# Kernel tuning notes

Hardware: AMD Instinct MI355X
Metric: run time of the kernel (lower is better)

Reference implementation:

```python
import jax, jax.numpy as jnp
import numpy as np

B, S, D, A_DIM = 8, 2048, 256, 64

def setup_inputs() -> dict:
    key = jax.random.key(0)
    k_x, k_wm, k_wl, k_eps = jax.random.split(key, 4)
    return {
        "x": jax.random.normal(k_x, (B, S, D), dtype=jnp.float32),
        "W_mean": jax.random.normal(k_wm, (D, A_DIM), dtype=jnp.float32) * (1.0 / np.sqrt(D)),
        "b_mean": jnp.zeros((A_DIM,), dtype=jnp.float32),
        "W_logvar": jax.random.normal(k_wl, (D, A_DIM), dtype=jnp.float32) * (1.0 / np.sqrt(D)),
        "b_logvar": jnp.zeros((A_DIM,), dtype=jnp.float32),
        "eps": jax.random.normal(k_eps, (B, S, A_DIM), dtype=jnp.float32),
    }

def reference(x, W_mean, b_mean, W_logvar, b_logvar, eps):
    d = x.shape[-1]
    scale = 1.0 / jnp.sqrt(jnp.asarray(d, dtype=x.dtype))
    # S_det = x x^T / sqrt(d)  -> [B, S, S]
    scores = jnp.einsum("bsd,btd->bst", x, x) * scale
    attn = jax.nn.softmax(scores, axis=-1)
    # A_det = softmax(S) x  -> [B, S, D]
    A_det = jnp.einsum("bst,btd->bsd", attn, x)
    A_mean = A_det @ W_mean + b_mean        # [B, S, A_DIM]
    A_logvar = A_det @ W_logvar + b_logvar  # [B, S, A_DIM]
    A = A_mean + jnp.exp(0.5 * A_logvar) * eps  # sqrt(exp(logvar)) = exp(logvar/2)
    return (A_mean, A_logvar, A)
```

## Files before the change

kernel.cpp:

```cpp
#include <hip/hip_runtime.h>

#define B_ 8
#define S_ 2048
#define D_ 256

typedef _Float16 f16;
typedef f16 f16x2 __attribute__((ext_vector_type(2)));
typedef f16 f16x8 __attribute__((ext_vector_type(8)));
typedef float f32x16 __attribute__((ext_vector_type(16)));
typedef unsigned int u32;
typedef u32 u32x4 __attribute__((ext_vector_type(4)));

typedef const __attribute__((address_space(1))) unsigned int* gptr_t;
typedef __attribute__((address_space(3))) unsigned int* lptr_t;

__device__ __forceinline__ void gload_lds16(const void* g, void* l) {
  __builtin_amdgcn_global_load_lds((gptr_t)(unsigned long long)g,
                                   (lptr_t)(unsigned long long)l, 16, 0, 0);
}

__device__ __forceinline__ u32 packf16(float a, float b) {
  f16x2 t; t[0] = (f16)a; t[1] = (f16)b;
  return __builtin_bit_cast(u32, t);
}

__device__ __forceinline__ void pack16(const f32x16& p, int hi, u32x4& o0, u32x4& o1) {
#pragma unroll
  for (int c2 = 0; c2 < 2; ++c2) {
    u32 a1 = packf16(p[8 * c2 + 0], p[8 * c2 + 1]);
    u32 a2 = packf16(p[8 * c2 + 2], p[8 * c2 + 3]);
    u32 b1 = packf16(p[8 * c2 + 4], p[8 * c2 + 5]);
    u32 b2 = packf16(p[8 * c2 + 6], p[8 * c2 + 7]);
    u32 xa1 = __shfl_xor(a1, 32), xa2 = __shfl_xor(a2, 32);
    u32 xb1 = __shfl_xor(b1, 32), xb2 = __shfl_xor(b2, 32);
    u32x4 f;
    f[0] = hi ? xb1 : a1;
    f[1] = hi ? xb2 : a2;
    f[2] = hi ? b1 : xa1;
    f[3] = hi ? b2 : xa2;
    if (c2) o1 = f; else o0 = f;
  }
}

#define SC2F 0.09016844f
#define NMAXR 20.0f

__global__ void prep(const float* __restrict__ x, const float* __restrict__ Wm,
                     const float* __restrict__ Wl, f16* __restrict__ xh,
                     float* __restrict__ n2, f16* __restrict__ Wt) {
  __shared__ f16 tile[64][264];
  const int bid = blockIdx.x;
  const int t = threadIdx.x;
  if (bid < 256) {
    const int b = bid >> 5, st = bid & 31;
    const int s0 = st * 64;
    const float* xb = x + ((size_t)(b * S_ + s0)) * D_;
    f16* xhb = xh + ((size_t)(b * S_ + s0)) * D_;
#pragma unroll
    for (int it = 0; it < 16; ++it) {
      int flat = it * 256 + t;
      int r = flat >> 6, c4 = flat & 63;
      float4 v = *reinterpret_cast<const float4*>(xb + r * 256 + c4 * 4);
      f16 h0 = (f16)v.x, h1 = (f16)v.y, h2 = (f16)v.z, h3 = (f16)v.w;
      f16x2 p0 = {h0, h1}, p1 = {h2, h3};
      uint2 wv; wv.x = __builtin_bit_cast(u32, p0); wv.y = __builtin_bit_cast(u32, p1);
      *reinterpret_cast<uint2*>(xhb + r * 256 + c4 * 4) = wv;
      tile[r][c4 * 4 + 0] = h0; tile[r][c4 * 4 + 1] = h1;
      tile[r][c4 * 4 + 2] = h2; tile[r][c4 * 4 + 3] = h3;
    }
    __syncthreads();
    {
      int r = t >> 2, qd = t & 3;
      float s = 0.0f;
#pragma unroll
      for (int i = 0; i < 8; ++i) {
        f16x8 v = *reinterpret_cast<const f16x8*>(&tile[r][qd * 64 + i * 8]);
#pragma unroll
        for (int u = 0; u < 8; ++u) { float f = (float)v[u]; s += f * f; }
      }
      s += __shfl_xor(s, 1); s += __shfl_xor(s, 2);
      if (qd == 0) n2[b * S_ + s0 + r] = s;
    }
  } else {
    int idx = (bid - 256) * 1024 + t * 4;
    int j = idx >> 8, d = idx & 255;
#pragma unroll
    for (int k2 = 0; k2 < 4; ++k2) {
      float v = (j < 64) ? Wm[(d + k2) * 64 + j] : Wl[(d + k2) * 64 + (j - 64)];
      Wt[idx + k2] = (f16)v;
    }
  }
}

__launch_bounds__(256)
__global__ void xw_kern(const f16* __restrict__ xh, const f16* __restrict__ Wt,
                        f16* __restrict__ XWt) {
  __shared__ f16 Ax[2][4096];
  __shared__ f16 Ww[2][8192];
  const int idx = blockIdx.x;
  const int b = idx & 7;
  const int sb = (idx >> 3) * 64;
  const int tid = threadIdx.x, lane = tid & 63, w = tid >> 6;
  const int l31 = lane & 31, hi = lane >> 5;
  const f16* xb = xh + (size_t)b * S_ * D_;

#define XW_STAGE(st, pp)                                                       \
  {                                                                            \
    _Pragma("unroll") for (int i = 0; i < 2; ++i) {                            \
      int ch = i * 256 + tid; int r = ch >> 3, c = ch & 7;                     \
      int csrc = c ^ (r & 7);                                                  \
      gload_lds16(xb + (size_t)(sb + r) * 256 + ((st) * 64) + csrc * 8,        \
                  &Ax[(pp)][0] + ch * 8);                                      \
    }                                                                          \
    _Pragma("unroll") for (int i = 0; i < 4; ++i) {                            \
      int ch = i * 256 + tid; int r = ch >> 3, c = ch & 7;                     \
      int csrc = c ^ (r & 7);                                                  \
      gload_lds16(Wt + (size_t)r * 256 + ((st) * 64) + csrc * 8,               \
                  &Ww[(pp)][0] + ch * 8);                                      \
    }                                                                          \
  }

  f32x16 acc[2];
#pragma unroll
  for (int i = 0; i < 2; ++i)
#pragma unroll
    for (int e = 0; e < 16; ++e) acc[i][e] = 0.0f;

  XW_STAGE(0, 0);
  __syncthreads();
#pragma unroll
  for (int t = 0; t < 4; ++t) {
    const int p = t & 1;
    if (t < 3) XW_STAGE(t + 1, p ^ 1);
#pragma unroll
    for (int kc = 0; kc < 4; ++kc) {
      int cc = ((2 * kc + hi) ^ (l31 & 7)) * 8;
      f16x8 bf = *reinterpret_cast<const f16x8*>(&Ww[p][(w * 32 + l31) * 64 + cc]);
#pragma unroll
      for (int mi = 0; mi < 2; ++mi) {
        f16x8 af = *reinterpret_cast<const f16x8*>(&Ax[p][(mi * 32 + l31) * 64 + cc]);
        acc[mi] = __builtin_amdgcn_mfma_f32_32x32x16_f16(af, bf, acc[mi], 0, 0, 0);
      }
    }
    __syncthreads();
  }
#undef XW_STAGE

  const int j = w * 32 + l31;
  f16* dst = XWt + ((size_t)b * 128 + j) * 2048;
#pragma unroll
  for (int mi = 0; mi < 2; ++mi) {
    u32x4 s0, s1;
    pack16(acc[mi], hi, s0, s1);
    *reinterpret_cast<u32x4*>(dst + sb + mi * 32 + hi * 8) = s0;
    *reinterpret_cast<u32x4*>(dst + sb + mi * 32 + 16 + hi * 8) = s1;
  }
}

__launch_bounds__(512, 4)
__global__ void gemm1_kern(const f16* __restrict__ xh, const float* __restrict__ n2,
                           f16* __restrict__ P, float* __restrict__ Lp,
                           int b0, int bm, int bsh) {
  __shared__ __align__(16) char smem[65536];
  f16* Aq = (f16*)smem;
  f16* Bk = (f16*)(smem + 32768);
  const int idx = blockIdx.x;
  const int bl = idx & bm;
  int tdec = idx >> bsh;
  int qt = 0;
#pragma unroll 1
  while (tdec >= 16 - qt) { tdec -= 16 - qt; ++qt; }
  const int kt = qt + tdec;
  const int b = b0 + bl;
  const int qb = qt * 128, kb = kt * 128;
  const int tid = threadIdx.x, lane = tid & 63, w = tid >> 6;
  const int l31 = lane & 31, hi = lane >> 5;
  const int wq = w >> 2, wk = w & 3;
  const f16* xb = xh + (size_t)b * S_ * D_;

#define G1_STAGE(st, pp)                                                       \
  { _Pragma("unroll") for (int i = 0; i < 4; ++i) {                            \
      int ii = w * 4 + i;                                                      \
      int flat = ii * 64 + lane;                                               \
      bool isB = ii >= 16;                                                     \
      int ch = isB ? flat - 1024 : flat;                                       \
      int r = ch >> 3, c = ch & 7;                                             \
      int csrc = c ^ (r & 7);                                                  \
      const f16* src = xb + (size_t)((isB ? kb : qb) + r) * 256 +              \
                       (st) * 64 + csrc * 8;                                   \
      f16* dst = (isB ? Bk : Aq) + ((pp) * 8192) + ch * 8;                     \
      gload_lds16(src, dst);                                                   \
    } }

  f32x16 acc[2];
#pragma unroll
  for (int i = 0; i < 2; ++i)
#pragma unroll
    for (int e = 0; e < 16; ++e) acc[i][e] = 0.0f;

  G1_STAGE(0, 0);
  __syncthreads();
#pragma unroll
  for (int t = 0; t < 4; ++t) {
    const int p = t & 1;
    if (t < 3) G1_STAGE(t + 1, p ^ 1);
#pragma unroll
    for (int kc = 0; kc < 4; ++kc) {
      int cc = ((2 * kc + hi) ^ (l31 & 7)) * 8;
      f16x8 af  = *reinterpret_cast<const f16x8*>(Bk + p * 8192 + (wk * 32 + l31) * 64 + cc);
      f16x8 bf0 = *reinterpret_cast<const f16x8*>(Aq + p * 8192 + (wq * 64 + l31) * 64 + cc);
      f16x8 bf1 = *reinterpret_cast<const f16x8*>(Aq + p * 8192 + (wq * 64 + 32 + l31) * 64 + cc);
      acc[0] = __builtin_amdgcn_mfma_f32_32x32x16_f16(af, bf0, acc[0], 0, 0, 0);
      acc[1] = __builtin_amdgcn_mfma_f32_32x32x16_f16(af, bf1, acc[1], 0, 0, 0);
    }
    __syncthreads();
  }
#undef G1_STAGE

  float* raw = (float*)smem;
  if (kt != qt) {
#pragma unroll
    for (int ni = 0; ni < 2; ++ni)
#pragma unroll
      for (int j = 0; j < 16; ++j) {
        int kvloc = wk * 32 + (j & 3) + 8 * (j >> 2) + 4 * hi;
        int qloc = wq * 64 + ni * 32 + l31;
        raw[kvloc * 128 + (qloc ^ ((kvloc & 7) << 2))] = acc[ni][j];
      }
  }

  float r2[2], lsum[2];
  int qrow[2];
#pragma unroll
  for (int ni = 0; ni < 2; ++ni) {
    qrow[ni] = qb + wq * 64 + ni * 32 + l31;
    r2[ni] = sqrtf(n2[b * S_ + qrow[ni]]) * (NMAXR * SC2F);
    lsum[ni] = 0.0f;
  }
#pragma unroll
  for (int ni = 0; ni < 2; ++ni)
#pragma unroll
    for (int j = 0; j < 16; ++j) {
      float v = exp2f(acc[ni][j] * SC2F - r2[ni]);
      acc[ni][j] = v;
      lsum[ni] += v;
    }
#pragma unroll
  for (int ni = 0; ni < 2; ++ni) lsum[ni] += __shfl_xor(lsum[ni], 32);

  const int colb = kb + wk * 32;
#pragma unroll
  for (int ni = 0; ni < 2; ++ni) {
    u32x4 s0, s1;
    pack16(acc[ni], hi, s0, s1);
    size_t rowp = (size_t)(bl * S_ + qrow[ni]) * 2048;
    *reinterpret_cast<u32x4*>(P + rowp + colb + hi * 8) = s0;
    *reinterpret_cast<u32x4*>(P + rowp + colb + 16 + hi * 8) = s1;
  }

  if (kt != qt) {
    __syncthreads();
    const int kvr = tid >> 2;
    const int qseg = (tid & 3) * 32;
    float r2kv = sqrtf(n2[b * S_ + kb + kvr]) * (NMAXR * SC2F);
    u32 ow[16];
    float tsum = 0.0f;
#pragma unroll
    for (int c8 = 0; c8 < 8; ++c8) {
      int qs = qseg + c8 * 4;
      float4 v = *reinterpret_cast<const float4*>(
          &raw[kvr * 128 + (qs ^ ((kvr & 7) << 2))]);
      float e0 = exp2f(v.x * SC2F - r2kv), e1 = exp2f(v.y * SC2F - r2kv);
      float e2 = exp2f(v.z * SC2F - r2kv), e3 = exp2f(v.w * SC2F - r2kv);
      tsum += (e0 + e1) + (e2 + e3);
      ow[c8 * 2 + 0] = packf16(e0, e1);
      ow[c8 * 2 + 1] = packf16(e2, e3);
    }
    size_t rowp = (size_t)(bl * S_ + kb + kvr) * 2048;
#pragma unroll
    for (int sseg = 0; sseg < 4; ++sseg) {
      u32x4 sv;
      sv[0] = ow[sseg * 4 + 0]; sv[1] = ow[sseg * 4 + 1];
      sv[2] = ow[sseg * 4 + 2]; sv[3] = ow[sseg * 4 + 3];
      *reinterpret_cast<u32x4*>(P + rowp + qb + qseg + sseg * 8) = sv;
    }
    tsum += __shfl_xor(tsum, 1);
    tsum += __shfl_xor(tsum, 2);
    if ((tid & 3) == 0)
      Lp[(size_t)(bl * 16 + qt) * 2048 + kb + kvr] = tsum;
  }

  __syncthreads();
  float* Lred = (float*)smem;
  if (hi == 0) {
    Lred[(wq * 64 + l31) * 4 + wk] = lsum[0];
    Lred[(wq * 64 + 32 + l31) * 4 + wk] = lsum[1];
  }
  __syncthreads();
  if (tid < 128) {
    float s = Lred[tid * 4] + Lred[tid * 4 + 1] + Lred[tid * 4 + 2] + Lred[tid * 4 + 3];
    Lp[(size_t)(bl * 16 + kt) * 2048 + qb + tid] = s;
  }
}

__launch_bounds__(256, 3)
__global__ void gemm2p_kern(const f16* __restrict__ P, const f16* __restrict__ XWt,
                            const float* __restrict__ Lp, const float* __restrict__ bm,
                            const float* __restrict__ bl_, const float* __restrict__ eps,
                            float* __restrict__ out, int b0, int bm_, int bsh) {
  __shared__ f16 Pq[2][4096];
  __shared__ f16 Xw[2][8192];
  const int idx = blockIdx.x;
  const int bl = idx & bm_;
  const int qt = idx >> bsh;
  const int b = b0 + bl;
  const int qb = qt * 64;
  const int tid = threadIdx.x, lane = tid & 63, w = tid >> 6;
  const int l31 = lane & 31, hi = lane >> 5;
  const int wq = w & 1, wc = w >> 1;
  const f16* xwb = XWt + (size_t)b * 128 * 2048;

#define GP_STAGE(tt, pp)                                                       \
  {                                                                            \
    _Pragma("unroll") for (int i = 0; i < 2; ++i) {                            \
      int ch = i * 256 + tid; int r = ch >> 3, c = ch & 7;                     \
      int csrc = c ^ (r & 7);                                                  \
      gload_lds16(P + (size_t)(bl * S_ + qb + r) * 2048 + ((tt) * 64) + csrc * 8, \
                  &Pq[(pp)][0] + ch * 8);                                      \
    }                                                                          \
    _Pragma("unroll") for (int i = 0; i < 4; ++i) {                            \
      int ch = i * 256 + tid; int r = ch >> 3, c = ch & 7;                     \
      int csrc = c ^ (r & 7);                                                  \
      gload_lds16(xwb + (size_t)r * 2048 + ((tt) * 64) + csrc * 8,             \
                  &Xw[(pp)][0] + ch * 8);                                      \
    }                                                                          \
  }

  f32x16 acc[2];
#pragma unroll
  for (int i = 0; i < 2; ++i)
#pragma unroll
    for (int e = 0; e < 16; ++e) acc[i][e] = 0.0f;

  GP_STAGE(0, 0);
  __syncthreads();
#pragma unroll 1
  for (int t = 0; t < 32; ++t) {
    const int p = t & 1;
    if (t < 31) GP_STAGE(t + 1, p ^ 1);
#pragma unroll
    for (int kc = 0; kc < 4; ++kc) {
      int cc = ((2 * kc + hi) ^ (l31 & 7)) * 8;
      f16x8 bf = *reinterpret_cast<const f16x8*>(&Pq[p][(wq * 32 + l31) * 64 + cc]);
#pragma unroll
      for (int mi = 0; mi < 2; ++mi) {
        int jrow = mi * 64 + wc * 32 + l31;
        f16x8 af = *reinterpret_cast<const f16x8*>(&Xw[p][jrow * 64 + cc]);
        acc[mi] = __builtin_amdgcn_mfma_f32_32x32x16_f16(af, bf, acc[mi], 0, 0, 0);
      }
    }
    __syncthreads();
  }
#undef GP_STAGE

  const int q = qb + wq * 32 + l31;
  const int grow = b * S_ + q;
  float L = 0.0f;
#pragma unroll
  for (int kt = 0; kt < 16; ++kt) L += Lp[(size_t)(bl * 16 + kt) * 2048 + q];
  float rL = 1.0f / L;
#pragma unroll
  for (int jg = 0; jg < 4; ++jg) {
    int cb = wc * 32 + 8 * jg + 4 * hi;
    float4 bmv = *reinterpret_cast<const float4*>(bm + cb);
    float4 blv = *reinterpret_cast<const float4*>(bl_ + cb);
    float4 ev  = *reinterpret_cast<const float4*>(eps + (size_t)grow * 64 + cb);
    float4 mn, lv, av;
    float* mnp = &mn.x; float* lvp = &lv.x; float* avp = &av.x;
    const float* bmp = &bmv.x; const float* blp = &blv.x; const float* evp = &ev.x;
#pragma unroll
    for (int jj = 0; jj < 4; ++jj) {
      int j = jg * 4 + jj;
      float m = acc[0][j] * rL + bmp[jj];
      float l = acc[1][j] * rL + blp[jj];
      mnp[jj] = m;
      lvp[jj] = l;
      avp[jj] = m + exp2f(0.7213475204f * l) * evp[jj];
    }
    float* o0 = out + (size_t)grow * 64 + cb;
    *reinterpret_cast<float4*>(o0) = mn;
    *reinterpret_cast<float4*>(o0 + 1048576) = lv;
    *reinterpret_cast<float4*>(o0 + 2097152) = av;
  }
}

extern "C" void kernel_launch(void* const* d_in, const int* in_sizes, int n_in,
                              void* d_out, int out_size, void* d_ws, size_t ws_size,
                              hipStream_t stream) {
  (void)in_sizes; (void)n_in; (void)out_size;
  const float* x   = (const float*)d_in[0];
  const float* Wm  = (const float*)d_in[1];
  const float* bmv = (const float*)d_in[2];
  const float* Wl  = (const float*)d_in[3];
  const float* blv = (const float*)d_in[4];
  const float* ep  = (const float*)d_in[5];
  float* out = (float*)d_out;

  char* ws = (char*)d_ws;
  f16*   xh   = (f16*)(ws + 0);
  f16*   XWt  = (f16*)(ws + 8388608);
  f16*   Wt   = (f16*)(ws + 12582912);
  float* n2   = (float*)(ws + 12648448);
  float* Lp   = (float*)(ws + 12713984);
  const size_t P_off = 13762560;
  f16*   Pbuf = (f16*)(ws + P_off);

  int bpp = 1;
  if      (ws_size >= P_off + (size_t)8 * 2048 * 2048 * 2) bpp = 8;
  else if (ws_size >= P_off + (size_t)4 * 2048 * 2048 * 2) bpp = 4;
  else if (ws_size >= P_off + (size_t)2 * 2048 * 2048 * 2) bpp = 2;
  const int bsh = (bpp == 8) ? 3 : (bpp == 4) ? 2 : (bpp == 2) ? 1 : 0;
  const int bm = bpp - 1;

  prep<<<288, 256, 0, stream>>>(x, Wm, Wl, xh, n2, Wt);
  xw_kern<<<256, 256, 0, stream>>>(xh, Wt, XWt);
  for (int b0 = 0; b0 < 8; b0 += bpp) {
    gemm1_kern<<<bpp * 136, 512, 0, stream>>>(xh, n2, Pbuf, Lp, b0, bm, bsh);
    gemm2p_kern<<<bpp * 32, 256, 0, stream>>>(Pbuf, XWt, Lp, bmv, blv, ep, out,
                                              b0, bm, bsh);
  }
  proj_dummy:;
}
```

Measured before the change: 75.90 us.

## Split gemm2 over the key dimension and add a reduction kernel

The P·XW GEMM now splits its 2048-long key dimension into two halves, doubling the number of blocks so more of the GPU is occupied. Each half writes normalized partial mean and logvar sums to a workspace buffer. A new reduce kernel adds the two partials, applies the biases, and computes the exp/eps output. This adds an extra launch, extra global traffic for the partials, and shifts the P buffer offset, which raises the workspace size needed for the larger batch-per-pass settings.

New measurement: 74.17 us. 1.02x faster.

```diff
diff --git a/kernel.cpp b/kernel.cpp
--- a/kernel.cpp
+++ b/kernel.cpp
@@ -305,16 +305,17 @@
 
 __launch_bounds__(256, 3)
 __global__ void gemm2p_kern(const f16* __restrict__ P, const f16* __restrict__ XWt,
-                            const float* __restrict__ Lp, const float* __restrict__ bm,
-                            const float* __restrict__ bl_, const float* __restrict__ eps,
-                            float* __restrict__ out, int b0, int bm_, int bsh) {
+                            const float* __restrict__ Lp, float* __restrict__ Yp,
+                            int b0, int bm_, int bsh, int kso) {
   __shared__ f16 Pq[2][4096];
   __shared__ f16 Xw[2][8192];
   const int idx = blockIdx.x;
   const int bl = idx & bm_;
-  const int qt = idx >> bsh;
+  const int qt = (idx >> bsh) & 31;
+  const int ks = idx >> (bsh + 5);
   const int b = b0 + bl;
   const int qb = qt * 64;
+  const int kcol0 = ks * 1024;
   const int tid = threadIdx.x, lane = tid & 63, w = tid >> 6;
   const int l31 = lane & 31, hi = lane >> 5;
   const int wq = w & 1, wc = w >> 1;
@@ -325,13 +326,13 @@
     _Pragma("unroll") for (int i = 0; i < 2; ++i) {                            \
       int ch = i * 256 + tid; int r = ch >> 3, c = ch & 7;                     \
       int csrc = c ^ (r & 7);                                                  \
-      gload_lds16(P + (size_t)(bl * S_ + qb + r) * 2048 + ((tt) * 64) + csrc * 8, \
+      gload_lds16(P + (size_t)(bl * S_ + qb + r) * 2048 + kcol0 + ((tt) * 64) + csrc * 8, \
                   &Pq[(pp)][0] + ch * 8);                                      \
     }                                                                          \
     _Pragma("unroll") for (int i = 0; i < 4; ++i) {                            \
       int ch = i * 256 + tid; int r = ch >> 3, c = ch & 7;                     \
       int csrc = c ^ (r & 7);                                                  \
-      gload_lds16(xwb + (size_t)r * 2048 + ((tt) * 64) + csrc * 8,             \
+      gload_lds16(xwb + (size_t)r * 2048 + kcol0 + ((tt) * 64) + csrc * 8,     \
                   &Xw[(pp)][0] + ch * 8);                                      \
     }                                                                          \
   }
@@ -345,9 +346,9 @@
   GP_STAGE(0, 0);
   __syncthreads();
 #pragma unroll 1
-  for (int t = 0; t < 32; ++t) {
+  for (int t = 0; t < 16; ++t) {
     const int p = t & 1;
-    if (t < 31) GP_STAGE(t + 1, p ^ 1);
+    if (t < 15) GP_STAGE(t + 1, p ^ 1);
 #pragma unroll
     for (int kc = 0; kc < 4; ++kc) {
       int cc = ((2 * kc + hi) ^ (l31 & 7)) * 8;
@@ -364,33 +365,64 @@
 #undef GP_STAGE
 
   const int q = qb + wq * 32 + l31;
-  const int grow = b * S_ + q;
   float L = 0.0f;
 #pragma unroll
   for (int kt = 0; kt < 16; ++kt) L += Lp[(size_t)(bl * 16 + kt) * 2048 + q];
   float rL = 1.0f / L;
+  float* dst = Yp + ((size_t)ks * kso + (size_t)bl * 2048 + q) * 128;
 #pragma unroll
   for (int jg = 0; jg < 4; ++jg) {
     int cb = wc * 32 + 8 * jg + 4 * hi;
-    float4 bmv = *reinterpret_cast<const float4*>(bm + cb);
-    float4 blv = *reinterpret_cast<const float4*>(bl_ + cb);
-    float4 ev  = *reinterpret_cast<const float4*>(eps + (size_t)grow * 64 + cb);
-    float4 mn, lv, av;
-    float* mnp = &mn.x; float* lvp = &lv.x; float* avp = &av.x;
-    const float* bmp = &bmv.x; const float* blp = &blv.x; const float* evp = &ev.x;
+    float4 mn, lv;
+    float* mnp = &mn.x; float* lvp = &lv.x;
 #pragma unroll
     for (int jj = 0; jj < 4; ++jj) {
       int j = jg * 4 + jj;
-      float m = acc[0][j] * rL + bmp[jj];
-      float l = acc[1][j] * rL + blp[jj];
-      mnp[jj] = m;
-      lvp[jj] = l;
-      avp[jj] = m + exp2f(0.7213475204f * l) * evp[jj];
-    }
-    float* o0 = out + (size_t)grow * 64 + cb;
-    *reinterpret_cast<float4*>(o0) = mn;
-    *reinterpret_cast<float4*>(o0 + 1048576) = lv;
-    *reinterpret_cast<float4*>(o0 + 2097152) = av;
+      mnp[jj] = acc[0][j] * rL;
+      lvp[jj] = acc[1][j] * rL;
+    }
+    *reinterpret_cast<float4*>(dst + cb) = mn;
+    *reinterpret_cast<float4*>(dst + 64 + cb) = lv;
+  }
+}
+
+__launch_bounds__(256)
+__global__ void reduce_kern(const float* __restrict__ Yp, const float* __restrict__ bm,
+                            const float* __restrict__ bl_, const float* __restrict__ eps,
+                            float* __restrict__ out, int b0, int kso) {
+  const int t = threadIdx.x;
+  const int rowp = blockIdx.x * 32 + (t >> 3);
+  const int j0 = (t & 7) * 8;
+  const int grow = b0 * 2048 + rowp;
+  const float* y0 = Yp + (size_t)rowp * 128;
+  const float* y1 = Yp + (size_t)kso * 128 + (size_t)rowp * 128;
+  float mv[8], lv[8], ev[8];
+#pragma unroll
+  for (int i = 0; i < 2; ++i) {
+    float4 a = *reinterpret_cast<const float4*>(y0 + j0 + i * 4);
+    float4 b = *reinterpret_cast<const float4*>(y1 + j0 + i * 4);
+    float4 c = *reinterpret_cast<const float4*>(y0 + 64 + j0 + i * 4);
+    float4 d = *reinterpret_cast<const float4*>(y1 + 64 + j0 + i * 4);
+    float4 e = *reinterpret_cast<const float4*>(eps + (size_t)grow * 64 + j0 + i * 4);
+    mv[i*4+0] = a.x + b.x; mv[i*4+1] = a.y + b.y; mv[i*4+2] = a.z + b.z; mv[i*4+3] = a.w + b.w;
+    lv[i*4+0] = c.x + d.x; lv[i*4+1] = c.y + d.y; lv[i*4+2] = c.z + d.z; lv[i*4+3] = c.w + d.w;
+    ev[i*4+0] = e.x; ev[i*4+1] = e.y; ev[i*4+2] = e.z; ev[i*4+3] = e.w;
+  }
+  float om[8], ol[8], oa[8];
+#pragma unroll
+  for (int i = 0; i < 8; ++i) {
+    float m = mv[i] + bm[j0 + i];
+    float l = lv[i] + bl_[j0 + i];
+    om[i] = m;
+    ol[i] = l;
+    oa[i] = m + exp2f(0.7213475204f * l) * ev[i];
+  }
+  float* o0 = out + (size_t)grow * 64 + j0;
+#pragma unroll
+  for (int i = 0; i < 2; ++i) {
+    *reinterpret_cast<float4*>(o0 + i * 4) = *reinterpret_cast<float4*>(&om[i * 4]);
+    *reinterpret_cast<float4*>(o0 + 1048576 + i * 4) = *reinterpret_cast<float4*>(&ol[i * 4]);
+    *reinterpret_cast<float4*>(o0 + 2097152 + i * 4) = *reinterpret_cast<float4*>(&oa[i * 4]);
   }
 }
 
@@ -412,7 +444,8 @@
   f16*   Wt   = (f16*)(ws + 12582912);
   float* n2   = (float*)(ws + 12648448);
   float* Lp   = (float*)(ws + 12713984);
-  const size_t P_off = 13762560;
+  float* Yp   = (float*)(ws + 13762560);
+  const size_t P_off = 30539776;
   f16*   Pbuf = (f16*)(ws + P_off);
 
   int bpp = 1;
@@ -421,13 +454,13 @@
   else if (ws_size >= P_off + (size_t)2 * 2048 * 2048 * 2) bpp = 2;
   const int bsh = (bpp == 8) ? 3 : (bpp == 4) ? 2 : (bpp == 2) ? 1 : 0;
   const int bm = bpp - 1;
+  const int kso = bpp * 2048;
 
   prep<<<288, 256, 0, stream>>>(x, Wm, Wl, xh, n2, Wt);
   xw_kern<<<256, 256, 0, stream>>>(xh, Wt, XWt);
   for (int b0 = 0; b0 < 8; b0 += bpp) {
     gemm1_kern<<<bpp * 136, 512, 0, stream>>>(xh, n2, Pbuf, Lp, b0, bm, bsh);
-    gemm2p_kern<<<bpp * 32, 256, 0, stream>>>(Pbuf, XWt, Lp, bmv, blv, ep, out,
-                                              b0, bm, bsh);
-  }
-  proj_dummy:;
-}
+    gemm2p_kern<<<bpp * 64, 256, 0, stream>>>(Pbuf, XWt, Lp, Yp, b0, bm, bsh, kso);
+    reduce_kern<<<bpp * 64, 256, 0, stream>>>(Yp, bmv, blv, ep, out, b0, kso);
+  }
+}
```
